# Kernel optimization log

Hardware: AMD Instinct MI355X
Metric: run time of the kernel (lower is better)

Reference implementation:

```python
import jax, jax.numpy as jnp
import numpy as np
from jax import lax

VEHICLE_LABELS = jnp.array([2, 3, 4, 6, 8], dtype=jnp.int64)
IMNET_MEAN = jnp.array([0.485, 0.456, 0.406], dtype=jnp.float32)
IMNET_STD = jnp.array([0.229, 0.224, 0.225], dtype=jnp.float32)
CROP = 64  # fixed RoIAlign output resolution replacing the variable-size python crop loop


def setup_inputs() -> dict:
    key = jax.random.key(0)
    ks = jax.random.split(key, 8)
    B, N, H, W = 8, 300, 512, 512
    x = jax.random.uniform(ks[0], (B, 3, H, W), dtype=jnp.float32)
    # well-formed boxes [x_min, y_min, x_max, y_max] inside the image
    tl = jax.random.uniform(ks[1], (B, N, 2), dtype=jnp.float32) * (W - 64.0)
    wh = jax.random.uniform(ks[2], (B, N, 2), dtype=jnp.float32) * 192.0 + 16.0
    br = jnp.minimum(tl + wh, float(W))
    boxes = jnp.concatenate([tl, br], axis=-1)  # [B,N,4]
    scores = jax.random.uniform(ks[3], (B, N), dtype=jnp.float32)
    labels = jax.random.randint(ks[4], (B, N), 0, 91).astype(jnp.int64)
    Wc = jax.random.normal(ks[5], (256, 3, 7, 7), dtype=jnp.float32) * 0.1
    bc = jnp.zeros((256,), dtype=jnp.float32)
    Wf = jax.random.normal(ks[6], (256, 4096), dtype=jnp.float32) / np.sqrt(256.0)
    bf = jnp.zeros((4096,), dtype=jnp.float32)
    return {"x": x, "boxes": boxes, "scores": scores, "labels": labels,
            "Wc": Wc, "bc": bc, "Wf": Wf, "bf": bf}


def extractor(imgs, Wc, bc, Wf, bf):
    # imgs [N,3,h,w] -> [N,4096]
    y = lax.conv_general_dilated(imgs, Wc, (4, 4), 'SAME',
                                 dimension_numbers=('NCHW', 'OIHW', 'NCHW'))
    y = jax.nn.relu(y + bc[None, :, None, None])
    y = y.mean(axis=(2, 3))  # global average pool -> [N,256]
    return y @ Wf + bf


def bilinear_sample(img, ys, xs):
    # img [C,H,W], ys [S], xs [S] -> [C,S,S]
    C, H, W = img.shape
    y0f = jnp.floor(ys); x0f = jnp.floor(xs)
    wy = (ys - y0f)[None, :, None]
    wx = (xs - x0f)[None, None, :]
    y0 = jnp.clip(y0f.astype(jnp.int32), 0, H - 1); y1 = jnp.clip(y0 + 1, 0, H - 1)
    x0 = jnp.clip(x0f.astype(jnp.int32), 0, W - 1); x1 = jnp.clip(x0 + 1, 0, W - 1)
    Ia = img[:, y0][:, :, x0]; Ib = img[:, y0][:, :, x1]
    Ic = img[:, y1][:, :, x0]; Id = img[:, y1][:, :, x1]
    return (Ia * (1 - wy) * (1 - wx) + Ib * (1 - wy) * wx
            + Ic * wy * (1 - wx) + Id * wy * wx)


def roi_align(img, box):
    # img [C,H,W], box [4] = x_min,y_min,x_max,y_max -> [C,CROP,CROP]
    t = (jnp.arange(CROP, dtype=img.dtype) + 0.5) / CROP
    ys = box[1] + t * (box[3] - box[1])
    xs = box[0] + t * (box[2] - box[0])
    return bilinear_sample(img, ys, xs)


def reference(x, boxes, scores, labels, Wc, bc, Wf, bf):
    score_threshold, K = 0.8, 20
    B = x.shape[0]
    # detection-weights transforms: ImageNet normalization
    images = (x - IMNET_MEAN[None, :, None, None]) / IMNET_STD[None, :, None, None]
    fullframe_features = extractor(images, Wc, bc, Wf, bf)  # [B,4096]
    # vehicle-class + score-threshold filtering, then top-k selection
    class_mask = (labels[..., None] == VEHICLE_LABELS[None, None, :]).any(-1)  # [B,N]
    comb_mask = class_mask & (scores > score_threshold)
    masked_scores = jnp.where(comb_mask, scores, -jnp.inf)
    vals, idx = lax.top_k(masked_scores, K)  # [B,K]
    valid = vals > -jnp.inf  # True where there is an object (matches torch code: 1=object)
    sel = jnp.take_along_axis(boxes, idx[..., None], axis=1)  # [B,K,4]
    Objects = jnp.where(valid[..., None], sel, 0.0)  # [B,K,4]
    # fused batched crop (RoIAlign) + batched extractor, replacing per-object loop
    crops = jax.vmap(lambda im, bxs: jax.vmap(lambda b: roi_align(im, b))(bxs))(images, Objects)  # [B,K,3,CROP,CROP]
    feats = extractor(crops.reshape(B * K, 3, CROP, CROP), Wc, bc, Wf, bf).reshape(B, K, 4096)
    degenerate = (Objects[..., 2] <= Objects[..., 0]) | (Objects[..., 3] <= Objects[..., 1])
    Object_features = jnp.where((valid & ~degenerate)[..., None], feats, 0.0)  # [B,K,4096]
    return Objects, Object_features, valid, fullframe_features
```

## Files before the change

kernel.cpp:

```cpp
#include <hip/hip_runtime.h>
#include <hip/hip_bf16.h>

#define OBJ_OFF   0
#define FEAT_OFF  640
#define VALID_OFF 656000
#define FF_OFF    656160

#define POOLED_N  (168 * 256)
#define SELBOX_N  (160 * 4)
#define FLAGS_N   (160)
#define K3        192

typedef __attribute__((ext_vector_type(8))) short short8v;
typedef __attribute__((ext_vector_type(4))) short short4v;
typedef __attribute__((ext_vector_type(4))) float f32x4;

__device__ __forceinline__ unsigned int rne_bf16(float f) {
    unsigned int u = __float_as_uint(f);
    return (u + 0x7FFFu + ((u >> 16) & 1u)) >> 16;
}

__global__ __launch_bounds__(256) void prep_kernel(
    const float* __restrict__ Wc, unsigned short* __restrict__ Wb)
{
    int i = blockIdx.x * 256 + threadIdx.x;
    int oc = i / K3, k = i % K3;
    int c = k >> 6, r = (k >> 3) & 7, q = k & 7;
    float v = (r < 7 && q < 7) ? Wc[oc * 147 + c * 49 + r * 7 + q] : 0.f;
    Wb[i] = (unsigned short)rne_bf16(v);
}

__global__ __launch_bounds__(512) void topk_kernel(
    const float* __restrict__ boxes, const float* __restrict__ scores,
    const int* __restrict__ labels, float* __restrict__ d_out,
    float* __restrict__ selbox, float* __restrict__ flags)
{
    __shared__ unsigned long long keys[512];
    __shared__ unsigned long long red[512];
    const int b = blockIdx.x, t = threadIdx.x;

    unsigned long long key = 0ULL;
    if (t < 300) {
        float s = scores[b * 300 + t];
        int   l = labels[b * 300 + t];
        bool cls = (l == 2) || (l == 3) || (l == 4) || (l == 6) || (l == 8);
        if (cls && s > 0.8f) {
            key = ((unsigned long long)__float_as_uint(s) << 32) |
                  (unsigned long long)(unsigned int)(~(unsigned int)t);
        }
    }
    keys[t] = key;
    __syncthreads();

    for (int k = 0; k < 20; ++k) {
        red[t] = keys[t];
        __syncthreads();
        for (int s = 256; s > 0; s >>= 1) {
            if (t < s) red[t] = (red[t] > red[t + s]) ? red[t] : red[t + s];
            __syncthreads();
        }
        unsigned long long m = red[0];
        const int slot = b * 20 + k;
        if (m == 0ULL) {
            if (t == 0) {
                d_out[OBJ_OFF + slot * 4 + 0] = 0.f;
                d_out[OBJ_OFF + slot * 4 + 1] = 0.f;
                d_out[OBJ_OFF + slot * 4 + 2] = 0.f;
                d_out[OBJ_OFF + slot * 4 + 3] = 0.f;
                d_out[VALID_OFF + slot] = 0.f;
                selbox[slot * 4 + 0] = 0.f; selbox[slot * 4 + 1] = 0.f;
                selbox[slot * 4 + 2] = 0.f; selbox[slot * 4 + 3] = 0.f;
                flags[slot] = 0.f;
            }
        } else if (keys[t] == m) {
            const float bx0 = boxes[(b * 300 + t) * 4 + 0];
            const float by0 = boxes[(b * 300 + t) * 4 + 1];
            const float bx1 = boxes[(b * 300 + t) * 4 + 2];
            const float by1 = boxes[(b * 300 + t) * 4 + 3];
            d_out[OBJ_OFF + slot * 4 + 0] = bx0;
            d_out[OBJ_OFF + slot * 4 + 1] = by0;
            d_out[OBJ_OFF + slot * 4 + 2] = bx1;
            d_out[OBJ_OFF + slot * 4 + 3] = by1;
            d_out[VALID_OFF + slot] = 1.f;
            selbox[slot * 4 + 0] = bx0; selbox[slot * 4 + 1] = by0;
            selbox[slot * 4 + 2] = bx1; selbox[slot * 4 + 3] = by1;
            bool deg = (bx1 <= bx0) || (by1 <= by0);
            flags[slot] = deg ? 0.f : 1.f;
            keys[t] = 0ULL;
        }
        __syncthreads();
    }
}

__device__ __forceinline__ void conv_core(
    const unsigned short (&tile)[3][20][68],
    const unsigned short* __restrict__ Wb, const float* __restrict__ bc,
    float* __restrict__ pooled, int prow, int tid)
{
    const int w = tid >> 6, l = tid & 63;
    const int lr = l & 15, lq = l >> 4;
    const int n0 = w * 64;

    f32x4 acc[4][4];
#pragma unroll
    for (int mf = 0; mf < 4; ++mf)
#pragma unroll
        for (int nf = 0; nf < 4; ++nf)
            acc[mf][nf] = (f32x4){0.f, 0.f, 0.f, 0.f};

#pragma unroll
    for (int ks = 0; ks < 6; ++ks) {
        const int kq = ks * 4 + lq;
        const int c = kq >> 3, rr = kq & 7;
        const int koff = ks * 32 + lq * 8;

        short8v a[4], bfr[4];
#pragma unroll
        for (int mf = 0; mf < 4; ++mf) {
            const unsigned short* ap = &tile[c][mf * 4 + rr][lr * 4];
            short4v a0 = *(const short4v*)ap;
            short4v a1 = *(const short4v*)(ap + 4);
            a[mf] = __builtin_shufflevector(a0, a1, 0, 1, 2, 3, 4, 5, 6, 7);
        }
#pragma unroll
        for (int nf = 0; nf < 4; ++nf)
            bfr[nf] = *(const short8v*)&Wb[(size_t)(n0 + nf * 16 + lr) * K3 + koff];
#pragma unroll
        for (int mf = 0; mf < 4; ++mf)
#pragma unroll
            for (int nf = 0; nf < 4; ++nf)
                acc[mf][nf] = __builtin_amdgcn_mfma_f32_16x16x32_bf16(
                    a[mf], bfr[nf], acc[mf][nf], 0, 0, 0);
    }

#pragma unroll
    for (int nf = 0; nf < 4; ++nf) {
        const int oc = n0 + nf * 16 + lr;
        const float bias = bc[oc];
        float s = 0.f;
#pragma unroll
        for (int mf = 0; mf < 4; ++mf)
#pragma unroll
            for (int r = 0; r < 4; ++r) {
                float pv = acc[mf][nf][r] + bias;
                s += pv > 0.f ? pv : 0.f;
            }
        s += __shfl_down(s, 32);
        s += __shfl_down(s, 16);
        if (l < 16) atomicAdd(&pooled[prow * 256 + oc], s);
    }
}

__global__ __launch_bounds__(256) void ffconv_mfma(
    const float* __restrict__ x, const unsigned short* __restrict__ Wb,
    const float* __restrict__ bc, float* __restrict__ pooled)
{
    __shared__ __align__(16) unsigned short tile[3][20][68];
    const int b = blockIdx.y;
    const int tile_y = blockIdx.x >> 3;
    const int tile_x = blockIdx.x & 7;
    const int tid = threadIdx.x;
    const int iy0 = tile_y * 16 - 1, ix0 = tile_x * 64 - 1;

    const float mean[3] = {0.485f, 0.456f, 0.406f};
    const float istd[3] = {1.0f / 0.229f, 1.0f / 0.224f, 1.0f / 0.225f};

    for (int i = tid; i < 3 * 20 * 68; i += 256) {
        int c = i / 1360, rem = i % 1360;
        int ir = rem / 68, icol = rem % 68;
        int gy = iy0 + ir, gx = ix0 + icol;
        float v = 0.f;
        if (gy >= 0 && gy < 512 && gx >= 0 && gx < 512)
            v = (x[((size_t)(b * 3 + c) * 512 + gy) * 512 + gx] - mean[c]) * istd[c];
        tile[c][ir][icol] = (unsigned short)rne_bf16(v);
    }
    __syncthreads();
    conv_core(tile, Wb, bc, pooled, b, tid);
}

__global__ __launch_bounds__(256) void cropconv_mfma(
    const float* __restrict__ x, const unsigned short* __restrict__ Wb,
    const float* __restrict__ bc, const float* __restrict__ selbox,
    const float* __restrict__ flags, float* __restrict__ pooled)
{
    const int bk = blockIdx.x >> 2, quarter = blockIdx.x & 3;
    if (flags[bk] == 0.f) return;
    const int b = bk / 20;
    const int tid = threadIdx.x;

    __shared__ __align__(16) unsigned short tile[3][20][68];

    const float bx0 = selbox[bk * 4 + 0], by0 = selbox[bk * 4 + 1];
    const float bx1 = selbox[bk * 4 + 2], by1 = selbox[bk * 4 + 3];
    const float sy = (by1 - by0) * (1.f / 64.f);
    const float sx = (bx1 - bx0) * (1.f / 64.f);

    const float mean[3] = {0.485f, 0.456f, 0.406f};
    const float istd[3] = {1.0f / 0.229f, 1.0f / 0.224f, 1.0f / 0.225f};
    const float* __restrict__ img = x + (size_t)b * 3 * 512 * 512;

    for (int i = tid; i < 3 * 20 * 68; i += 256) {
        int c = i / 1360, rem = i % 1360;
        int ir = rem / 68, icol = rem % 68;
        int cy = quarter * 16 - 1 + ir;
        int cx = icol - 1;
        float v = 0.f;
        if (cy >= 0 && cy < 64 && cx >= 0 && cx < 64) {
            float ys = by0 + ((float)cy + 0.5f) * sy;
            float xs = bx0 + ((float)cx + 0.5f) * sx;
            float yf = floorf(ys), xf = floorf(xs);
            float wy = ys - yf, wx = xs - xf;
            int iy0 = min(max((int)yf, 0), 511), iy1 = min(iy0 + 1, 511);
            int ix0 = min(max((int)xf, 0), 511), ix1 = min(ix0 + 1, 511);
            const float* ch = img + (size_t)c * 512 * 512;
            float Ia = ch[iy0 * 512 + ix0], Ib = ch[iy0 * 512 + ix1];
            float Ic = ch[iy1 * 512 + ix0], Id = ch[iy1 * 512 + ix1];
            float s = Ia * (1.f - wy) * (1.f - wx) + Ib * (1.f - wy) * wx +
                      Ic * wy * (1.f - wx) + Id * wy * wx;
            v = (s - mean[c]) * istd[c];
        }
        tile[c][ir][icol] = (unsigned short)rne_bf16(v);
    }
    __syncthreads();
    conv_core(tile, Wb, bc, pooled, 8 + bk, tid);
}

__global__ __launch_bounds__(256) void fc_kernel(
    const float* __restrict__ pooled, const float* __restrict__ Wf,
    const float* __restrict__ bf, const float* __restrict__ flags,
    float* __restrict__ d_out)
{
    __shared__ __align__(16) float p[24][64];
    const int cb = blockIdx.x, rg = blockIdx.y, kz = blockIdx.z;
    const int tid = threadIdx.x;

    for (int i = tid; i < 24 * 64; i += 256) {
        int r = i >> 6, k = i & 63;
        int R = rg * 24 + r;
        float s = (R < 8) ? (1.f / 16384.f) : (1.f / 256.f);
        p[r][k] = pooled[R * 256 + kz * 64 + k] * s;
    }
    __syncthreads();

    float acc[24];
#pragma unroll
    for (int r = 0; r < 24; ++r) acc[r] = 0.f;

    const int col = cb * 256 + tid;
    const float* wp = Wf + (size_t)(kz * 64) * 4096 + col;
    for (int k = 0; k < 64; k += 4) {
        float w0 = wp[(size_t)(k + 0) * 4096];
        float w1 = wp[(size_t)(k + 1) * 4096];
        float w2 = wp[(size_t)(k + 2) * 4096];
        float w3 = wp[(size_t)(k + 3) * 4096];
#pragma unroll
        for (int r = 0; r < 24; ++r) {
            float4 pv = *(const float4*)&p[r][k];
            acc[r] += pv.x * w0 + pv.y * w1 + pv.z * w2 + pv.w * w3;
        }
    }

    const float bias_on = (kz == 0) ? 1.f : 0.f;
#pragma unroll
    for (int r = 0; r < 24; ++r) {
        int R = rg * 24 + r;
        float v = acc[r] + bias_on * bf[col];
        if (R < 8) {
            atomicAdd(&d_out[FF_OFF + R * 4096 + col], v);
        } else {
            int rr = R - 8;
            if (flags[rr] != 0.f)
                atomicAdd(&d_out[FEAT_OFF + rr * 4096 + col], v);
        }
    }
}

extern "C" void kernel_launch(void* const* d_in, const int* in_sizes, int n_in,
                              void* d_out, int out_size, void* d_ws, size_t ws_size,
                              hipStream_t stream)
{
    const float* x      = (const float*)d_in[0];
    const float* boxes  = (const float*)d_in[1];
    const float* scores = (const float*)d_in[2];
    const int*   labels = (const int*)d_in[3];
    const float* Wc     = (const float*)d_in[4];
    const float* bc     = (const float*)d_in[5];
    const float* Wf     = (const float*)d_in[6];
    const float* bf     = (const float*)d_in[7];
    float* out = (float*)d_out;

    float* pooled = (float*)d_ws;
    float* selbox = pooled + POOLED_N;
    float* flags  = selbox + SELBOX_N;
    unsigned short* Wb = (unsigned short*)(flags + FLAGS_N);

    hipMemsetAsync(d_ws, 0, POOLED_N * sizeof(float), stream);
    hipMemsetAsync(d_out, 0, (size_t)out_size * sizeof(float), stream);

    prep_kernel<<<K3, 256, 0, stream>>>(Wc, Wb);
    topk_kernel<<<8, 512, 0, stream>>>(boxes, scores, labels, out, selbox, flags);
    ffconv_mfma<<<dim3(256, 8), 256, 0, stream>>>(x, Wb, bc, pooled);
    cropconv_mfma<<<640, 256, 0, stream>>>(x, Wb, bc, selbox, flags, pooled);
    fc_kernel<<<dim3(16, 7, 4), 256, 0, stream>>>(pooled, Wf, bf, flags, out);
}
```

Before: 190.4 us.

## Double-buffer full-frame conv tiles with register-resident weights and batched crop gathers

The full-frame conv kernel now has each block process four row tiles. It keeps the bf16 weight fragments and bias in registers and double-buffers the LDS input tile, so the global loads for the next tile are in flight while MFMA runs on the current one. Pooled sums are accumulated in registers and issue one atomic per block instead of one per tile. The crop kernel batches its bilinear gathers into register arrays to get more memory-level parallelism, and zeroing of the pooled buffer moves into prep_kernel to drop a memset. The cost is higher register pressure (launch_bounds 256,2) and a full-frame grid four times smaller.

```diff
diff --git a/kernel.cpp b/kernel.cpp
--- a/kernel.cpp
+++ b/kernel.cpp
@@ -21,9 +21,11 @@
 }
 
 __global__ __launch_bounds__(256) void prep_kernel(
-    const float* __restrict__ Wc, unsigned short* __restrict__ Wb)
+    const float* __restrict__ Wc, unsigned short* __restrict__ Wb,
+    float* __restrict__ pooled)
 {
     int i = blockIdx.x * 256 + threadIdx.x;
+    if (i < POOLED_N) pooled[i] = 0.f;
     int oc = i / K3, k = i % K3;
     int c = k >> 6, r = (k >> 3) & 7, q = k & 7;
     float v = (r < 7 && q < 7) ? Wc[oc * 147 + c * 49 + r * 7 + q] : 0.f;
@@ -92,6 +94,140 @@
     }
 }
 
+__device__ __forceinline__ void conv_compute_regB(
+    const unsigned short (&tb)[3][20][68], const short8v (&breg)[6][4],
+    const float (&bias)[4], float (&poolacc)[4], int lr, int lq)
+{
+    f32x4 acc[4][4];
+#pragma unroll
+    for (int mf = 0; mf < 4; ++mf)
+#pragma unroll
+        for (int nf = 0; nf < 4; ++nf)
+            acc[mf][nf] = (f32x4){0.f, 0.f, 0.f, 0.f};
+
+#pragma unroll
+    for (int ks = 0; ks < 6; ++ks) {
+        const int kq = ks * 4 + lq;
+        const int c = kq >> 3, rr = kq & 7;
+        short8v a[4];
+#pragma unroll
+        for (int mf = 0; mf < 4; ++mf) {
+            const unsigned short* ap = &tb[c][mf * 4 + rr][lr * 4];
+            short4v a0 = *(const short4v*)ap;
+            short4v a1 = *(const short4v*)(ap + 4);
+            a[mf] = __builtin_shufflevector(a0, a1, 0, 1, 2, 3, 4, 5, 6, 7);
+        }
+#pragma unroll
+        for (int mf = 0; mf < 4; ++mf)
+#pragma unroll
+            for (int nf = 0; nf < 4; ++nf)
+                acc[mf][nf] = __builtin_amdgcn_mfma_f32_16x16x32_bf16(
+                    a[mf], breg[ks][nf], acc[mf][nf], 0, 0, 0);
+    }
+
+#pragma unroll
+    for (int nf = 0; nf < 4; ++nf) {
+        float s = 0.f;
+#pragma unroll
+        for (int mf = 0; mf < 4; ++mf)
+#pragma unroll
+            for (int r = 0; r < 4; ++r) {
+                float pv = acc[mf][nf][r] + bias[nf];
+                s += pv > 0.f ? pv : 0.f;
+            }
+        poolacc[nf] += s;
+    }
+}
+
+__device__ __forceinline__ void ff_stage_issue(
+    const float* __restrict__ img, int iy0, int ix0, int tid, float (&sv)[16])
+{
+#pragma unroll
+    for (int it = 0; it < 16; ++it) {
+        int i = tid + it * 256;
+        float v = 0.f;
+        if (i < 4080) {
+            int c = i / 1360, rem = i % 1360;
+            int ir = rem / 68, icol = rem % 68;
+            int gy = iy0 + ir, gx = ix0 + icol;
+            if (gy >= 0 && gy < 512 && gx >= 0 && gx < 512)
+                v = img[((size_t)c * 512 + gy) * 512 + gx];
+        }
+        sv[it] = v;
+    }
+}
+
+__device__ __forceinline__ void ff_stage_write(
+    unsigned short (&tb)[3][20][68], int iy0, int ix0, int tid,
+    const float (&sv)[16], const float* mean, const float* istd)
+{
+#pragma unroll
+    for (int it = 0; it < 16; ++it) {
+        int i = tid + it * 256;
+        if (i < 4080) {
+            int c = i / 1360, rem = i % 1360;
+            int ir = rem / 68, icol = rem % 68;
+            int gy = iy0 + ir, gx = ix0 + icol;
+            bool inb = (gy >= 0 && gy < 512 && gx >= 0 && gx < 512);
+            float nv = inb ? (sv[it] - mean[c]) * istd[c] : 0.f;
+            ((unsigned short*)tb)[i] = (unsigned short)rne_bf16(nv);
+        }
+    }
+}
+
+__global__ __launch_bounds__(256, 2) void ffconv_mfma(
+    const float* __restrict__ x, const unsigned short* __restrict__ Wb,
+    const float* __restrict__ bc, float* __restrict__ pooled)
+{
+    __shared__ __align__(16) unsigned short buf[2][3][20][68];
+    const int b = blockIdx.y;
+    const int tile_x = blockIdx.x & 7, rblk = blockIdx.x >> 3;
+    const int tid = threadIdx.x;
+    const int w = tid >> 6, l = tid & 63, lr = l & 15, lq = l >> 4;
+    const int n0 = w * 64;
+    const int ix0 = tile_x * 64 - 1;
+
+    const float mean[3] = {0.485f, 0.456f, 0.406f};
+    const float istd[3] = {1.0f / 0.229f, 1.0f / 0.224f, 1.0f / 0.225f};
+    const float* __restrict__ img = x + (size_t)b * 3 * 512 * 512;
+
+    short8v breg[6][4];
+#pragma unroll
+    for (int ks = 0; ks < 6; ++ks)
+#pragma unroll
+        for (int nf = 0; nf < 4; ++nf)
+            breg[ks][nf] = *(const short8v*)&Wb[(size_t)(n0 + nf * 16 + lr) * K3 + ks * 32 + lq * 8];
+
+    float bias[4];
+#pragma unroll
+    for (int nf = 0; nf < 4; ++nf) bias[nf] = bc[n0 + nf * 16 + lr];
+
+    float poolacc[4] = {0.f, 0.f, 0.f, 0.f};
+    float sv[16];
+
+    ff_stage_issue(img, (rblk * 4 + 0) * 16 - 1, ix0, tid, sv);
+    ff_stage_write(buf[0], (rblk * 4 + 0) * 16 - 1, ix0, tid, sv, mean, istd);
+    __syncthreads();
+
+#pragma unroll
+    for (int q = 0; q < 4; ++q) {
+        const int cur = q & 1;
+        if (q < 3) ff_stage_issue(img, (rblk * 4 + q + 1) * 16 - 1, ix0, tid, sv);
+        conv_compute_regB(buf[cur], breg, bias, poolacc, lr, lq);
+        if (q < 3)
+            ff_stage_write(buf[cur ^ 1], (rblk * 4 + q + 1) * 16 - 1, ix0, tid, sv, mean, istd);
+        __syncthreads();
+    }
+
+#pragma unroll
+    for (int nf = 0; nf < 4; ++nf) {
+        float s = poolacc[nf];
+        s += __shfl_down(s, 32);
+        s += __shfl_down(s, 16);
+        if (l < 16) atomicAdd(&pooled[b * 256 + n0 + nf * 16 + lr], s);
+    }
+}
+
 __device__ __forceinline__ void conv_core(
     const unsigned short (&tile)[3][20][68],
     const unsigned short* __restrict__ Wb, const float* __restrict__ bc,
@@ -151,34 +287,7 @@
     }
 }
 
-__global__ __launch_bounds__(256) void ffconv_mfma(
-    const float* __restrict__ x, const unsigned short* __restrict__ Wb,
-    const float* __restrict__ bc, float* __restrict__ pooled)
-{
-    __shared__ __align__(16) unsigned short tile[3][20][68];
-    const int b = blockIdx.y;
-    const int tile_y = blockIdx.x >> 3;
-    const int tile_x = blockIdx.x & 7;
-    const int tid = threadIdx.x;
-    const int iy0 = tile_y * 16 - 1, ix0 = tile_x * 64 - 1;
-
-    const float mean[3] = {0.485f, 0.456f, 0.406f};
-    const float istd[3] = {1.0f / 0.229f, 1.0f / 0.224f, 1.0f / 0.225f};
-
-    for (int i = tid; i < 3 * 20 * 68; i += 256) {
-        int c = i / 1360, rem = i % 1360;
-        int ir = rem / 68, icol = rem % 68;
-        int gy = iy0 + ir, gx = ix0 + icol;
-        float v = 0.f;
-        if (gy >= 0 && gy < 512 && gx >= 0 && gx < 512)
-            v = (x[((size_t)(b * 3 + c) * 512 + gy) * 512 + gx] - mean[c]) * istd[c];
-        tile[c][ir][icol] = (unsigned short)rne_bf16(v);
-    }
-    __syncthreads();
-    conv_core(tile, Wb, bc, pooled, b, tid);
-}
-
-__global__ __launch_bounds__(256) void cropconv_mfma(
+__global__ __launch_bounds__(256, 2) void cropconv_mfma(
     const float* __restrict__ x, const unsigned short* __restrict__ Wb,
     const float* __restrict__ bc, const float* __restrict__ selbox,
     const float* __restrict__ flags, float* __restrict__ pooled)
@@ -199,27 +308,49 @@
     const float istd[3] = {1.0f / 0.229f, 1.0f / 0.224f, 1.0f / 0.225f};
     const float* __restrict__ img = x + (size_t)b * 3 * 512 * 512;
 
-    for (int i = tid; i < 3 * 20 * 68; i += 256) {
-        int c = i / 1360, rem = i % 1360;
-        int ir = rem / 68, icol = rem % 68;
-        int cy = quarter * 16 - 1 + ir;
-        int cx = icol - 1;
-        float v = 0.f;
-        if (cy >= 0 && cy < 64 && cx >= 0 && cx < 64) {
-            float ys = by0 + ((float)cy + 0.5f) * sy;
-            float xs = bx0 + ((float)cx + 0.5f) * sx;
-            float yf = floorf(ys), xf = floorf(xs);
-            float wy = ys - yf, wx = xs - xf;
-            int iy0 = min(max((int)yf, 0), 511), iy1 = min(iy0 + 1, 511);
-            int ix0 = min(max((int)xf, 0), 511), ix1 = min(ix0 + 1, 511);
-            const float* ch = img + (size_t)c * 512 * 512;
-            float Ia = ch[iy0 * 512 + ix0], Ib = ch[iy0 * 512 + ix1];
-            float Ic = ch[iy1 * 512 + ix0], Id = ch[iy1 * 512 + ix1];
-            float s = Ia * (1.f - wy) * (1.f - wx) + Ib * (1.f - wy) * wx +
-                      Ic * wy * (1.f - wx) + Id * wy * wx;
-            v = (s - mean[c]) * istd[c];
-        }
-        tile[c][ir][icol] = (unsigned short)rne_bf16(v);
+#pragma unroll
+    for (int rd = 0; rd < 2; ++rd) {
+        float rva[8], rvb[8], rvc[8], rvd[8], rwy[8], rwx[8];
+#pragma unroll
+        for (int e = 0; e < 8; ++e) {
+            int i = tid + (rd * 8 + e) * 256;
+            float Ia = 0.f, Ib = 0.f, Ic = 0.f, Id = 0.f, wy = 0.f, wx = 0.f;
+            if (i < 4080) {
+                int c = i / 1360, rem = i % 1360;
+                int ir = rem / 68, icol = rem % 68;
+                int cy = quarter * 16 - 1 + ir, cx = icol - 1;
+                if (cy >= 0 && cy < 64 && cx >= 0 && cx < 64) {
+                    float ys = by0 + ((float)cy + 0.5f) * sy;
+                    float xs = bx0 + ((float)cx + 0.5f) * sx;
+                    float yf = floorf(ys), xf = floorf(xs);
+                    wy = ys - yf; wx = xs - xf;
+                    int iy0 = min(max((int)yf, 0), 511), iy1 = min(iy0 + 1, 511);
+                    int ix0 = min(max((int)xf, 0), 511), ix1 = min(ix0 + 1, 511);
+                    const float* ch = img + (size_t)c * 512 * 512;
+                    Ia = ch[iy0 * 512 + ix0]; Ib = ch[iy0 * 512 + ix1];
+                    Ic = ch[iy1 * 512 + ix0]; Id = ch[iy1 * 512 + ix1];
+                }
+            }
+            rva[e] = Ia; rvb[e] = Ib; rvc[e] = Ic; rvd[e] = Id;
+            rwy[e] = wy; rwx[e] = wx;
+        }
+#pragma unroll
+        for (int e = 0; e < 8; ++e) {
+            int i = tid + (rd * 8 + e) * 256;
+            if (i < 4080) {
+                int c = i / 1360, rem = i % 1360;
+                int ir = rem / 68, icol = rem % 68;
+                int cy = quarter * 16 - 1 + ir, cx = icol - 1;
+                float v = 0.f;
+                if (cy >= 0 && cy < 64 && cx >= 0 && cx < 64) {
+                    float wy = rwy[e], wx = rwx[e];
+                    float s = rva[e] * (1.f - wy) * (1.f - wx) + rvb[e] * (1.f - wy) * wx +
+                              rvc[e] * wy * (1.f - wx) + rvd[e] * wy * wx;
+                    v = (s - mean[c]) * istd[c];
+                }
+                ((unsigned short*)tile)[i] = (unsigned short)rne_bf16(v);
+            }
+        }
     }
     __syncthreads();
     conv_core(tile, Wb, bc, pooled, 8 + bk, tid);
@@ -294,12 +425,11 @@
     float* flags  = selbox + SELBOX_N;
     unsigned short* Wb = (unsigned short*)(flags + FLAGS_N);
 
-    hipMemsetAsync(d_ws, 0, POOLED_N * sizeof(float), stream);
     hipMemsetAsync(d_out, 0, (size_t)out_size * sizeof(float), stream);
 
-    prep_kernel<<<K3, 256, 0, stream>>>(Wc, Wb);
+    prep_kernel<<<K3, 256, 0, stream>>>(Wc, Wb, pooled);
     topk_kernel<<<8, 512, 0, stream>>>(boxes, scores, labels, out, selbox, flags);
-    ffconv_mfma<<<dim3(256, 8), 256, 0, stream>>>(x, Wb, bc, pooled);
+    ffconv_mfma<<<dim3(64, 8), 256, 0, stream>>>(x, Wb, bc, pooled);
     cropconv_mfma<<<640, 256, 0, stream>>>(x, Wb, bc, selbox, flags, pooled);
     fc_kernel<<<dim3(16, 7, 4), 256, 0, stream>>>(pooled, Wf, bf, flags, out);
 }
```

New measurement: 228.3 us. 1.2x slower.
